# Kernel tuning notes

Hardware: AMD Instinct MI355X
Metric: run time of the kernel (lower is better)

Reference implementation:

```python
import jax, jax.numpy as jnp
import numpy as np

SCALE = 0.08838834764831845  # 1/sqrt(head_dim=128)

T, H, D = 8192, 16, 128
NUM_SLOTS = 16384
SEQ_LEN = 2048


def setup_inputs() -> dict:
    key = jax.random.key(0)
    kq, kk, kv = jax.random.split(key, 3)
    q = jax.random.normal(kq, (T, H, D), dtype=jnp.float32)
    k = jax.random.normal(kk, (T, H, D), dtype=jnp.float32)
    v = jax.random.normal(kv, (T, H, D), dtype=jnp.float32)
    k_cache = jnp.zeros((NUM_SLOTS, H * D), dtype=jnp.float32)
    v_cache = jnp.zeros((NUM_SLOTS, H * D), dtype=jnp.float32)
    slot_mapping = jnp.arange(T, dtype=jnp.int32)  # contiguous slots; -1 would mean skip
    return {"q": q, "k": k, "v": v, "k_cache": k_cache, "v_cache": v_cache,
            "slot_mapping": slot_mapping, "seq_len": SEQ_LEN}


def reference(q, k, v, k_cache, v_cache, slot_mapping, seq_len):
    # --- store_kvcache: scatter per-token K/V rows into paged cache slots ---
    t, h, d = q.shape
    num_slots = k_cache.shape[0]
    # slot == -1 means "do not store"; remap to an out-of-bounds index and drop.
    safe_slots = jnp.where(slot_mapping < 0, num_slots, slot_mapping)
    k_cache = k_cache.at[safe_slots].set(k.reshape(t, h * d), mode="drop")
    v_cache = v_cache.at[safe_slots].set(v.reshape(t, h * d), mode="drop")

    # --- prefill attention reading K/V from the cache (block_tables path) ---
    # cu_seqlens = [0, S, 2S, ...]: equal-length sequences packed contiguously,
    # so the per-sequence cache slices are the first t rows reshaped to [B,S,H,D].
    b = t // seq_len
    qb = q.reshape(b, seq_len, h, d)
    kb = k_cache[:t].reshape(b, seq_len, h, d)
    vb = v_cache[:t].reshape(b, seq_len, h, d)

    scores = jnp.einsum("bqhd,bkhd->bhqk", qb, kb) * SCALE  # [B,H,S,S]
    causal = jnp.tril(jnp.ones((seq_len, seq_len), dtype=bool))
    scores = jnp.where(causal[None, None], scores, -jnp.inf)
    p = jax.nn.softmax(scores, axis=-1)
    o = jnp.einsum("bhqk,bkhd->bqhd", p, vb)
    return o.reshape(t, h, d)
```

## Files before the change

kernel.cpp:

```cpp
#include <hip/hip_runtime.h>

typedef float f32x16 __attribute__((ext_vector_type(16)));
typedef __bf16 bf16x8 __attribute__((ext_vector_type(8)));
typedef unsigned int uint2v __attribute__((ext_vector_type(2)));

#define Hh 16
#define Dd 128
#define SEQ 2048
#define HD 2048
#define ATT_C 0.12751743f
#define NEGINF (-__builtin_inff())

__device__ __forceinline__ ushort f2bf(float f) {
    uint u = __builtin_bit_cast(uint, f);
    return (ushort)((u + 0x7FFFu + ((u >> 16) & 1u)) >> 16);
}

__device__ __forceinline__ uint4 pack8(float4 a, float4 b) {
    uint4 u;
    u.x = (uint)f2bf(a.x) | ((uint)f2bf(a.y) << 16);
    u.y = (uint)f2bf(a.z) | ((uint)f2bf(a.w) << 16);
    u.z = (uint)f2bf(b.x) | ((uint)f2bf(b.y) << 16);
    u.w = (uint)f2bf(b.z) | ((uint)f2bf(b.w) << 16);
    return u;
}

__device__ __forceinline__ uint cvtpk(float a, float b) {
    uint r;
    asm("v_cvt_pk_bf16_f32 %0, %1, %2" : "=v"(r) : "v"(a), "v"(b));
    return r;
}

__device__ __forceinline__ f32x16 zero16() {
    f32x16 v;
#pragma unroll
    for (int i = 0; i < 16; ++i) v[i] = 0.f;
    return v;
}

__device__ __forceinline__ float hsum16(const f32x16 v) {
    float a0 = v[0] + v[1], a1 = v[2] + v[3], a2 = v[4] + v[5], a3 = v[6] + v[7];
    float a4 = v[8] + v[9], a5 = v[10] + v[11], a6 = v[12] + v[13], a7 = v[14] + v[15];
    float b0 = a0 + a1, b1 = a2 + a3, b2 = a4 + a5, b3 = a6 + a7;
    return (b0 + b1) + (b2 + b3);
}

__device__ __forceinline__ void gll16(const void* g, void* l) {
    __builtin_amdgcn_global_load_lds(
        (const __attribute__((address_space(1))) unsigned int*)g,
        (__attribute__((address_space(3))) unsigned int*)l, 16, 0, 0);
}

__device__ __forceinline__ bf16x8 mkfrag(uint a01, uint a23, uint a45, uint a67, int hi) {
    uint4 u;
#if __has_builtin(__builtin_amdgcn_permlane32_swap)
    uint2v xz = __builtin_amdgcn_permlane32_swap(a01, a45, false, false);
    uint2v yw = __builtin_amdgcn_permlane32_swap(a23, a67, false, false);
    u.x = xz[0]; u.y = yw[0]; u.z = xz[1]; u.w = yw[1];
    (void)hi;
#else
    uint s01 = __shfl_xor(a01, 32), s23 = __shfl_xor(a23, 32);
    uint s45 = __shfl_xor(a45, 32), s67 = __shfl_xor(a67, 32);
    u.x = hi ? s45 : a01;
    u.y = hi ? s67 : a23;
    u.z = hi ? a45 : s01;
    u.w = hi ? a67 : s23;
#endif
    return __builtin_bit_cast(bf16x8, u);
}

__global__ void buildinv(const int* __restrict__ slots, int* __restrict__ inv, int T) {
    int t = blockIdx.x * 256 + threadIdx.x;
    if (t < T) { int s = slots[t]; if (s >= 0 && s < T) inv[s] = t; }
}

__global__ void fusekv(const float* __restrict__ k, const float* __restrict__ v,
                       const float* __restrict__ kc, const float* __restrict__ vc,
                       const int* __restrict__ inv, ushort* __restrict__ ek,
                       ushort* __restrict__ evt) {
    __shared__ int sv[64];
    __shared__ ushort Ks[64][136];
    __shared__ ushort Lt[128][72];
    const int tid = threadIdx.x;
    const int r0 = blockIdx.x * 64, h = blockIdx.y;
    const int b = r0 >> 11, tok0 = r0 & (SEQ - 1);
    const long tb = ((long)(b * Hh + h) * 32 + (tok0 >> 6)) * 8192;
    if (tid < 64) sv[tid] = inv[r0 + tid];
    __syncthreads();
#pragma unroll
    for (int i = 0; i < 4; ++i) {
        int idx = i * 256 + tid, r = idx >> 4, sg = idx & 15;
        int s = sv[r];
        const float* src = (s >= 0 ? k + (long)s * HD : kc + (long)(r0 + r) * HD) + h * Dd + sg * 8;
        float4 A = *(const float4*)src;
        float4 Bv = *(const float4*)(src + 4);
        *(uint4*)&Ks[r][sg * 8] = pack8(A, Bv);
    }
    const int d = tid & 127, hf2 = tid >> 7;
#pragma unroll
    for (int i = 0; i < 8; ++i) {
        const int t = i * 8 + hf2 * 4;
        ushort wv[4];
#pragma unroll
        for (int jj = 0; jj < 4; ++jj) {
            int s = sv[t + jj];
            const float* sp = (s >= 0 ? v + (long)s * HD : vc + (long)(r0 + t + jj) * HD) + h * Dd + d;
            wv[jj] = f2bf(*sp);
        }
        uint2 u;
        u.x = (uint)wv[0] | ((uint)wv[1] << 16);
        u.y = (uint)wv[2] | ((uint)wv[3] << 16);
        *(uint2*)&Lt[d][t] = u;
    }
    __syncthreads();
#pragma unroll
    for (int i = 0; i < 4; ++i) {
        int c = i * 256 + tid, l = c & 31, j = (c >> 5) & 15, hf = c >> 9;
        *(uint4*)(ek + tb + (long)c * 8) = *(const uint4*)&Ks[hf * 32 + l][j * 8];
    }
#pragma unroll
    for (int i = 0; i < 4; ++i) {
        int c = i * 256 + tid, l = c & 31, ch = (c >> 5) & 7, nt = c >> 8;
        *(uint4*)(evt + tb + (long)c * 8) = *(const uint4*)&Lt[nt * 32 + l][ch * 8];
    }
}

#define DOHALF(HH)                                                                         \
  {                                                                                        \
    f32x16 za = zero16(), zb = zero16();                                                   \
    __builtin_amdgcn_s_setprio(1);                                                         \
    _Pragma("unroll")                                                                      \
    for (int kk = 0; kk < 4; ++kk) {                                                       \
      za = __builtin_amdgcn_mfma_f32_32x32x16_bf16(                                        \
          *(const bf16x8*)&Kb[(HH) * 4096 + kk * 512 + koff], qf[kk], za, 0, 0, 0);        \
      zb = __builtin_amdgcn_mfma_f32_32x32x16_bf16(                                        \
          *(const bf16x8*)&Kb[(HH) * 4096 + (kk + 4) * 512 + koff], qf[kk + 4], zb, 0, 0, 0); \
    }                                                                                      \
    __builtin_amdgcn_s_setprio(0);                                                         \
    f32x16 z = za + zb;                                                                    \
    const int kb0 = kv0 + (HH) * 32;                                                       \
    if (kb0 + 31 > qtb) {                                                                  \
      _Pragma("unroll")                                                                    \
      for (int r = 0; r < 16; ++r) {                                                       \
        const int kr = kb0 + ((r & 3) + 8 * (r >> 2) + 4 * hi);                            \
        z[r] = (kr <= qpos) ? z[r] : NEGINF;                                               \
      }                                                                                    \
    }                                                                                      \
    _Pragma("unroll")                                                                      \
    for (int r = 0; r < 16; ++r) z[r] = __builtin_amdgcn_exp2f(z[r]);                      \
    lsum += hsum16(z);                                                                     \
    bf16x8 pa0 = mkfrag(cvtpk(z[0], z[1]), cvtpk(z[2], z[3]),                              \
                        cvtpk(z[4], z[5]), cvtpk(z[6], z[7]), hi);                         \
    bf16x8 pa1 = mkfrag(cvtpk(z[8], z[9]), cvtpk(z[10], z[11]),                            \
                        cvtpk(z[12], z[13]), cvtpk(z[14], z[15]), hi);                     \
    __builtin_amdgcn_s_setprio(1);                                                         \
    _Pragma("unroll")                                                                      \
    for (int nt = 0; nt < 4; ++nt) {                                                       \
      const int vb = nt * 2048 + koff + (HH) * 1024;                                       \
      o[nt] = __builtin_amdgcn_mfma_f32_32x32x16_bf16(pa0, *(const bf16x8*)&Vb[vb], o[nt], 0, 0, 0);       \
      o[nt] = __builtin_amdgcn_mfma_f32_32x32x16_bf16(pa1, *(const bf16x8*)&Vb[vb + 512], o[nt], 0, 0, 0); \
    }                                                                                      \
    __builtin_amdgcn_s_setprio(0);                                                         \
  }

__global__ __launch_bounds__(512) void attn32(const float* __restrict__ q,
                                              const ushort* __restrict__ ek,
                                              const ushort* __restrict__ evt,
                                              float* __restrict__ out) {
    __shared__ ushort KV[2][16384];

    const int tid = threadIdx.x;
    const int w = tid >> 6, lane = tid & 63;
    const int l31 = lane & 31, hi = lane >> 5;
    const int g = blockIdx.x;
    const int bh = g & 63;
    const int jj = 7 - (g >> 6);
    const int b = bh >> 4, h = bh & 15;
    const int ns = 4 * (jj + 1);
    const long kvbase = (long)bh * 32 * 8192;
    const int koff = hi * 256 + l31 * 8;
    const int qtb = jj * 256 + w * 32;
    const int qpos = qtb + l31;

    bf16x8 qf[8];
    {
        const float* qp = q + ((long)(b * SEQ + qtb + l31) * Hh + h) * Dd + hi * 8;
#pragma unroll
        for (int kk = 0; kk < 8; ++kk) {
            float4 A = *(const float4*)(qp + kk * 16);
            float4 Bv = *(const float4*)(qp + kk * 16 + 4);
            A.x *= ATT_C; A.y *= ATT_C; A.z *= ATT_C; A.w *= ATT_C;
            Bv.x *= ATT_C; Bv.y *= ATT_C; Bv.z *= ATT_C; Bv.w *= ATT_C;
            union { uint4 u; bf16x8 v; } cv;
            cv.u = pack8(A, Bv);
            qf[kk] = cv.v;
        }
    }
    auto stage = [&](int nb, int t) {
        const ushort* kg = ek + kvbase + (long)t * 8192 + tid * 8;
        const ushort* vg = evt + kvbase + (long)t * 8192 + tid * 8;
        ushort* kl = &KV[nb][tid * 8];
        ushort* vl = &KV[nb][8192 + tid * 8];
#pragma unroll
        for (int i = 0; i < 2; ++i) {
            gll16(kg + i * 4096, kl + i * 4096);
            gll16(vg + i * 4096, vl + i * 4096);
        }
    };

    f32x16 o[4];
#pragma unroll
    for (int nt = 0; nt < 4; ++nt) o[nt] = zero16();
    float lsum = 0.f;

    stage(0, 0);
    __syncthreads();

    int cur = 0;
    for (int s = 0; s < ns; ++s) {
        if (s + 1 < ns) stage(cur ^ 1, s + 1);
        const int kv0 = s * 64;
        const ushort* Kb = &KV[cur][0];
        const ushort* Vb = &KV[cur][8192];

        if (kv0 <= qtb + 31) {
            DOHALF(0);
            if (kv0 + 32 <= qtb + 31) DOHALF(1);
        }

        __syncthreads();
        cur ^= 1;
    }

    const float lt = lsum + __shfl_xor(lsum, 32);
    const float inv_ = 1.f / lt;
#pragma unroll
    for (int r = 0; r < 16; ++r) {
        const int qr = (r & 3) + 8 * (r >> 2) + 4 * hi;
        const float ivr = __shfl(inv_, qr);
        float* op = out + ((long)(b * SEQ + qtb + qr) * Hh + h) * Dd + l31;
        op[0]  = o[0][r] * ivr;
        op[32] = o[1][r] * ivr;
        op[64] = o[2][r] * ivr;
        op[96] = o[3][r] * ivr;
    }
}

extern "C" void kernel_launch(void* const* d_in, const int* in_sizes, int n_in,
                              void* d_out, int out_size, void* d_ws, size_t ws_size,
                              hipStream_t stream) {
    const float* q = (const float*)d_in[0];
    const float* k = (const float*)d_in[1];
    const float* v = (const float*)d_in[2];
    const float* k_cache = (const float*)d_in[3];
    const float* v_cache = (const float*)d_in[4];
    const int* slot_mapping = (const int*)d_in[5];
    float* out = (float*)d_out;

    const int T = in_sizes[0] / HD;
    (void)n_in; (void)out_size; (void)ws_size;

    ushort* ek = (ushort*)d_ws;
    ushort* evt = ek + (size_t)T * HD;
    int* inv = (int*)(evt + (size_t)T * HD);

    hipMemsetAsync(inv, 0xFF, (size_t)T * sizeof(int), stream);
    buildinv<<<T / 256, 256, 0, stream>>>(slot_mapping, inv, T);
    fusekv<<<dim3(T / 64, Hh), 256, 0, stream>>>(k, v, k_cache, v_cache, inv, ek, evt);
    attn32<<<dim3(512), 512, 0, stream>>>(q, ek, evt, out);
}
```

Baseline: 142.7 us.

## Double KV tile per pipeline stage to 128 keys and interleave block scheduling

Each loop iteration now stages and processes 128 keys (two 64-key subtiles) per double-buffered step instead of 64, halving the number of __syncthreads barriers and stage issues. LDS usage doubles to 128 KB per block, which may reduce occupancy. Block-to-query-tile mapping also changes from strictly heaviest-first to a heavy/light interleave across waves of blocks, to balance the causal workload.

```diff
diff --git a/kernel.cpp b/kernel.cpp
--- a/kernel.cpp
+++ b/kernel.cpp
@@ -125,8 +125,10 @@
     }
 }
 
-#define DOHALF(HH)                                                                         \
+#define DOQ(SUB, HH)                                                                       \
   {                                                                                        \
+    const ushort* Kb = &KV[cur][(SUB) * 16384];                                            \
+    const ushort* Vb = &KV[cur][(SUB) * 16384 + 8192];                                     \
     f32x16 za = zero16(), zb = zero16();                                                   \
     __builtin_amdgcn_s_setprio(1);                                                         \
     _Pragma("unroll")                                                                      \
@@ -138,7 +140,7 @@
     }                                                                                      \
     __builtin_amdgcn_s_setprio(0);                                                         \
     f32x16 z = za + zb;                                                                    \
-    const int kb0 = kv0 + (HH) * 32;                                                       \
+    const int kb0 = kv0 + (SUB) * 64 + (HH) * 32;                                          \
     if (kb0 + 31 > qtb) {                                                                  \
       _Pragma("unroll")                                                                    \
       for (int r = 0; r < 16; ++r) {                                                       \
@@ -167,16 +169,17 @@
                                               const ushort* __restrict__ ek,
                                               const ushort* __restrict__ evt,
                                               float* __restrict__ out) {
-    __shared__ ushort KV[2][16384];
+    __shared__ ushort KV[2][32768];
 
     const int tid = threadIdx.x;
     const int w = tid >> 6, lane = tid & 63;
     const int l31 = lane & 31, hi = lane >> 5;
     const int g = blockIdx.x;
     const int bh = g & 63;
-    const int jj = 7 - (g >> 6);
+    const int u_ = g >> 6;
+    const int jj = (u_ < 4) ? 7 - u_ : u_ - 4;
     const int b = bh >> 4, h = bh & 15;
-    const int ns = 4 * (jj + 1);
+    const int ns = 2 * (jj + 1);
     const long kvbase = (long)bh * 32 * 8192;
     const int koff = hi * 256 + l31 * 8;
     const int qtb = jj * 256 + w * 32;
@@ -191,20 +194,24 @@
             float4 Bv = *(const float4*)(qp + kk * 16 + 4);
             A.x *= ATT_C; A.y *= ATT_C; A.z *= ATT_C; A.w *= ATT_C;
             Bv.x *= ATT_C; Bv.y *= ATT_C; Bv.z *= ATT_C; Bv.w *= ATT_C;
-            union { uint4 u; bf16x8 v; } cv;
-            cv.u = pack8(A, Bv);
+            union { uint4 uu; bf16x8 v; } cv;
+            cv.uu = pack8(A, Bv);
             qf[kk] = cv.v;
         }
     }
-    auto stage = [&](int nb, int t) {
-        const ushort* kg = ek + kvbase + (long)t * 8192 + tid * 8;
-        const ushort* vg = evt + kvbase + (long)t * 8192 + tid * 8;
-        ushort* kl = &KV[nb][tid * 8];
-        ushort* vl = &KV[nb][8192 + tid * 8];
-#pragma unroll
-        for (int i = 0; i < 2; ++i) {
-            gll16(kg + i * 4096, kl + i * 4096);
-            gll16(vg + i * 4096, vl + i * 4096);
+    auto stage = [&](int nb, int sp) {
+        const long tbase = kvbase + (long)sp * 16384;
+#pragma unroll
+        for (int sub = 0; sub < 2; ++sub) {
+            const ushort* kg = ek + tbase + sub * 8192 + tid * 8;
+            const ushort* vg = evt + tbase + sub * 8192 + tid * 8;
+            ushort* kl = &KV[nb][sub * 16384 + tid * 8];
+            ushort* vl = &KV[nb][sub * 16384 + 8192 + tid * 8];
+#pragma unroll
+            for (int i = 0; i < 2; ++i) {
+                gll16(kg + i * 4096, kl + i * 4096);
+                gll16(vg + i * 4096, vl + i * 4096);
+            }
         }
     };
 
@@ -219,13 +226,15 @@
     int cur = 0;
     for (int s = 0; s < ns; ++s) {
         if (s + 1 < ns) stage(cur ^ 1, s + 1);
-        const int kv0 = s * 64;
-        const ushort* Kb = &KV[cur][0];
-        const ushort* Vb = &KV[cur][8192];
+        const int kv0 = s * 128;
 
         if (kv0 <= qtb + 31) {
-            DOHALF(0);
-            if (kv0 + 32 <= qtb + 31) DOHALF(1);
+            DOQ(0, 0);
+            if (kv0 + 32 <= qtb + 31) DOQ(0, 1);
+            if (kv0 + 64 <= qtb + 31) {
+                DOQ(1, 0);
+                if (kv0 + 96 <= qtb + 31) DOQ(1, 1);
+            }
         }
 
         __syncthreads();
```

After: 157.3 us. +10.2%, slower.

## Split KV tile across warp pairs and halve query tile per block

Applied to the files above, without the earlier changes.

Each block now handles 128 query rows instead of 256, with the 8 warps split into 4 query sub-tiles times 2 KV halves of each 64-key stage. The two partial outputs and row sums are combined through shared memory at the end. This doubles the grid to 1024 blocks to improve load balance and occupancy across CUs for the causal triangle, at the cost of an extra shared-memory reduction and reloading K/V tiles in more blocks.

```diff
diff --git a/kernel.cpp b/kernel.cpp
--- a/kernel.cpp
+++ b/kernel.cpp
@@ -125,62 +125,28 @@
     }
 }
 
-#define DOHALF(HH)                                                                         \
-  {                                                                                        \
-    f32x16 za = zero16(), zb = zero16();                                                   \
-    __builtin_amdgcn_s_setprio(1);                                                         \
-    _Pragma("unroll")                                                                      \
-    for (int kk = 0; kk < 4; ++kk) {                                                       \
-      za = __builtin_amdgcn_mfma_f32_32x32x16_bf16(                                        \
-          *(const bf16x8*)&Kb[(HH) * 4096 + kk * 512 + koff], qf[kk], za, 0, 0, 0);        \
-      zb = __builtin_amdgcn_mfma_f32_32x32x16_bf16(                                        \
-          *(const bf16x8*)&Kb[(HH) * 4096 + (kk + 4) * 512 + koff], qf[kk + 4], zb, 0, 0, 0); \
-    }                                                                                      \
-    __builtin_amdgcn_s_setprio(0);                                                         \
-    f32x16 z = za + zb;                                                                    \
-    const int kb0 = kv0 + (HH) * 32;                                                       \
-    if (kb0 + 31 > qtb) {                                                                  \
-      _Pragma("unroll")                                                                    \
-      for (int r = 0; r < 16; ++r) {                                                       \
-        const int kr = kb0 + ((r & 3) + 8 * (r >> 2) + 4 * hi);                            \
-        z[r] = (kr <= qpos) ? z[r] : NEGINF;                                               \
-      }                                                                                    \
-    }                                                                                      \
-    _Pragma("unroll")                                                                      \
-    for (int r = 0; r < 16; ++r) z[r] = __builtin_amdgcn_exp2f(z[r]);                      \
-    lsum += hsum16(z);                                                                     \
-    bf16x8 pa0 = mkfrag(cvtpk(z[0], z[1]), cvtpk(z[2], z[3]),                              \
-                        cvtpk(z[4], z[5]), cvtpk(z[6], z[7]), hi);                         \
-    bf16x8 pa1 = mkfrag(cvtpk(z[8], z[9]), cvtpk(z[10], z[11]),                            \
-                        cvtpk(z[12], z[13]), cvtpk(z[14], z[15]), hi);                     \
-    __builtin_amdgcn_s_setprio(1);                                                         \
-    _Pragma("unroll")                                                                      \
-    for (int nt = 0; nt < 4; ++nt) {                                                       \
-      const int vb = nt * 2048 + koff + (HH) * 1024;                                       \
-      o[nt] = __builtin_amdgcn_mfma_f32_32x32x16_bf16(pa0, *(const bf16x8*)&Vb[vb], o[nt], 0, 0, 0);       \
-      o[nt] = __builtin_amdgcn_mfma_f32_32x32x16_bf16(pa1, *(const bf16x8*)&Vb[vb + 512], o[nt], 0, 0, 0); \
-    }                                                                                      \
-    __builtin_amdgcn_s_setprio(0);                                                         \
-  }
-
 __global__ __launch_bounds__(512) void attn32(const float* __restrict__ q,
                                               const ushort* __restrict__ ek,
                                               const ushort* __restrict__ evt,
                                               float* __restrict__ out) {
     __shared__ ushort KV[2][16384];
+    __shared__ float Lsum[64];
 
     const int tid = threadIdx.x;
     const int w = tid >> 6, lane = tid & 63;
     const int l31 = lane & 31, hi = lane >> 5;
+    const int qsub = w & 3, kh = w >> 2;
     const int g = blockIdx.x;
     const int bh = g & 63;
-    const int jj = 7 - (g >> 6);
+    const int t = 15 - (g >> 6);
     const int b = bh >> 4, h = bh & 15;
-    const int ns = 4 * (jj + 1);
+    const int ns = 2 * (t + 1);
     const long kvbase = (long)bh * 32 * 8192;
     const int koff = hi * 256 + l31 * 8;
-    const int qtb = jj * 256 + w * 32;
+    const int qtb = t * 128 + qsub * 32;
     const int qpos = qtb + l31;
+    const int kof2 = kh * 4096;
+    const int vof2 = kh * 1024;
 
     bf16x8 qf[8];
     {
@@ -196,9 +162,9 @@
             qf[kk] = cv.v;
         }
     }
-    auto stage = [&](int nb, int t) {
-        const ushort* kg = ek + kvbase + (long)t * 8192 + tid * 8;
-        const ushort* vg = evt + kvbase + (long)t * 8192 + tid * 8;
+    auto stage = [&](int nb, int ti) {
+        const ushort* kg = ek + kvbase + (long)ti * 8192 + tid * 8;
+        const ushort* vg = evt + kvbase + (long)ti * 8192 + tid * 8;
         ushort* kl = &KV[nb][tid * 8];
         ushort* vl = &KV[nb][8192 + tid * 8];
 #pragma unroll
@@ -220,12 +186,46 @@
     for (int s = 0; s < ns; ++s) {
         if (s + 1 < ns) stage(cur ^ 1, s + 1);
         const int kv0 = s * 64;
-        const ushort* Kb = &KV[cur][0];
+        const ushort* Kb = &KV[cur][kof2];
         const ushort* Vb = &KV[cur][8192];
 
-        if (kv0 <= qtb + 31) {
-            DOHALF(0);
-            if (kv0 + 32 <= qtb + 31) DOHALF(1);
+        if (kv0 + kh * 32 <= qtb + 31) {
+            f32x16 za = zero16(), zb = zero16();
+            __builtin_amdgcn_s_setprio(1);
+#pragma unroll
+            for (int kk = 0; kk < 4; ++kk) {
+                za = __builtin_amdgcn_mfma_f32_32x32x16_bf16(
+                    *(const bf16x8*)&Kb[kk * 512 + koff], qf[kk], za, 0, 0, 0);
+                zb = __builtin_amdgcn_mfma_f32_32x32x16_bf16(
+                    *(const bf16x8*)&Kb[(kk + 4) * 512 + koff], qf[kk + 4], zb, 0, 0, 0);
+            }
+            __builtin_amdgcn_s_setprio(0);
+            f32x16 z = za + zb;
+            const int kb0 = kv0 + kh * 32;
+            if (kb0 + 31 > qtb) {
+#pragma unroll
+                for (int r = 0; r < 16; ++r) {
+                    const int kr = kb0 + ((r & 3) + 8 * (r >> 2) + 4 * hi);
+                    z[r] = (kr <= qpos) ? z[r] : NEGINF;
+                }
+            }
+#pragma unroll
+            for (int r = 0; r < 16; ++r) z[r] = __builtin_amdgcn_exp2f(z[r]);
+            lsum += hsum16(z);
+            bf16x8 pa0 = mkfrag(cvtpk(z[0], z[1]), cvtpk(z[2], z[3]),
+                                cvtpk(z[4], z[5]), cvtpk(z[6], z[7]), hi);
+            bf16x8 pa1 = mkfrag(cvtpk(z[8], z[9]), cvtpk(z[10], z[11]),
+                                cvtpk(z[12], z[13]), cvtpk(z[14], z[15]), hi);
+            __builtin_amdgcn_s_setprio(1);
+#pragma unroll
+            for (int nt = 0; nt < 4; ++nt) {
+                const int vb = nt * 2048 + koff + vof2;
+                o[nt] = __builtin_amdgcn_mfma_f32_32x32x16_bf16(
+                    pa0, *(const bf16x8*)&Vb[vb], o[nt], 0, 0, 0);
+                o[nt] = __builtin_amdgcn_mfma_f32_32x32x16_bf16(
+                    pa1, *(const bf16x8*)&Vb[vb + 512], o[nt], 0, 0, 0);
+            }
+            __builtin_amdgcn_s_setprio(0);
         }
 
         __syncthreads();
@@ -233,16 +233,34 @@
     }
 
     const float lt = lsum + __shfl_xor(lsum, 32);
-    const float inv_ = 1.f / lt;
-#pragma unroll
-    for (int r = 0; r < 16; ++r) {
-        const int qr = (r & 3) + 8 * (r >> 2) + 4 * hi;
-        const float ivr = __shfl(inv_, qr);
-        float* op = out + ((long)(b * SEQ + qtb + qr) * Hh + h) * Dd + l31;
-        op[0]  = o[0][r] * ivr;
-        op[32] = o[1][r] * ivr;
-        op[64] = o[2][r] * ivr;
-        op[96] = o[3][r] * ivr;
+    float* Ox = (float*)&KV[0][0];
+#pragma unroll
+    for (int ph = 0; ph < 2; ++ph) {
+        __syncthreads();
+        if (kh == 1 && (qsub >> 1) == ph) {
+            float* dst = Ox + (qsub & 1) * 4096 + lane;
+#pragma unroll
+            for (int nt = 0; nt < 4; ++nt)
+#pragma unroll
+                for (int r = 0; r < 16; ++r) dst[(nt * 16 + r) * 64] = o[nt][r];
+            if (lane < 32) Lsum[(qsub & 1) * 32 + lane] = lt;
+        }
+        __syncthreads();
+        if (kh == 0 && (qsub >> 1) == ph) {
+            const float* src = Ox + (qsub & 1) * 4096 + lane;
+            const float lt1 = Lsum[(qsub & 1) * 32 + l31];
+            const float inv_ = 1.f / (lt + lt1);
+#pragma unroll
+            for (int r = 0; r < 16; ++r) {
+                const int qr = (r & 3) + 8 * (r >> 2) + 4 * hi;
+                const float ivr = __shfl(inv_, qr);
+                float* op = out + ((long)(b * SEQ + qtb + qr) * Hh + h) * Dd + l31;
+                op[0]  = (o[0][r] + src[(0 * 16 + r) * 64]) * ivr;
+                op[32] = (o[1][r] + src[(1 * 16 + r) * 64]) * ivr;
+                op[64] = (o[2][r] + src[(2 * 16 + r) * 64]) * ivr;
+                op[96] = (o[3][r] + src[(3 * 16 + r) * 64]) * ivr;
+            }
+        }
     }
 }
 
@@ -267,5 +285,5 @@
     hipMemsetAsync(inv, 0xFF, (size_t)T * sizeof(int), stream);
     buildinv<<<T / 256, 256, 0, stream>>>(slot_mapping, inv, T);
     fusekv<<<dim3(T / 64, Hh), 256, 0, stream>>>(k, v, k_cache, v_cache, inv, ek, evt);
-    attn32<<<dim3(512), 512, 0, stream>>>(q, ek, evt, out);
-}
+    attn32<<<dim3(1024), 512, 0, stream>>>(q, ek, evt, out);
+}
```

Result: slower. 181.6 us (+27.3%).

## Give each wave two 32-row query tiles to reuse K/V fragments

Applied to the files above, without the earlier changes.

Each wave now handles 64 query rows as two 32-row tiles instead of one, so every K and V fragment read from LDS feeds two MFMAs. Blocks shrink from 512 to 256 threads with launch bounds (256,2), and staging is adjusted so 256 threads still load the same 64-key tile. The aim is to halve LDS reads per MFMA and cut the number of waves sharing each staged tile. In exchange, registers roughly double for Q fragments and accumulators, which can lower occupancy, and causal masking gets coarser per wave, so some work in diagonal blocks is wasted.

```diff
diff --git a/kernel.cpp b/kernel.cpp
--- a/kernel.cpp
+++ b/kernel.cpp
@@ -127,46 +127,57 @@
 
 #define DOHALF(HH)                                                                         \
   {                                                                                        \
-    f32x16 za = zero16(), zb = zero16();                                                   \
+    f32x16 z0 = zero16(), z1 = zero16();                                                   \
     __builtin_amdgcn_s_setprio(1);                                                         \
     _Pragma("unroll")                                                                      \
-    for (int kk = 0; kk < 4; ++kk) {                                                       \
-      za = __builtin_amdgcn_mfma_f32_32x32x16_bf16(                                        \
-          *(const bf16x8*)&Kb[(HH) * 4096 + kk * 512 + koff], qf[kk], za, 0, 0, 0);        \
-      zb = __builtin_amdgcn_mfma_f32_32x32x16_bf16(                                        \
-          *(const bf16x8*)&Kb[(HH) * 4096 + (kk + 4) * 512 + koff], qf[kk + 4], zb, 0, 0, 0); \
+    for (int kk = 0; kk < 8; ++kk) {                                                       \
+      bf16x8 kf = *(const bf16x8*)&Kb[(HH) * 4096 + kk * 512 + koff];                      \
+      z0 = __builtin_amdgcn_mfma_f32_32x32x16_bf16(kf, qf0[kk], z0, 0, 0, 0);              \
+      z1 = __builtin_amdgcn_mfma_f32_32x32x16_bf16(kf, qf1[kk], z1, 0, 0, 0);              \
     }                                                                                      \
     __builtin_amdgcn_s_setprio(0);                                                         \
-    f32x16 z = za + zb;                                                                    \
     const int kb0 = kv0 + (HH) * 32;                                                       \
     if (kb0 + 31 > qtb) {                                                                  \
       _Pragma("unroll")                                                                    \
       for (int r = 0; r < 16; ++r) {                                                       \
         const int kr = kb0 + ((r & 3) + 8 * (r >> 2) + 4 * hi);                            \
-        z[r] = (kr <= qpos) ? z[r] : NEGINF;                                               \
+        z0[r] = (kr <= qp0) ? z0[r] : NEGINF;                                              \
+        z1[r] = (kr <= qp1) ? z1[r] : NEGINF;                                              \
       }                                                                                    \
     }                                                                                      \
     _Pragma("unroll")                                                                      \
-    for (int r = 0; r < 16; ++r) z[r] = __builtin_amdgcn_exp2f(z[r]);                      \
-    lsum += hsum16(z);                                                                     \
-    bf16x8 pa0 = mkfrag(cvtpk(z[0], z[1]), cvtpk(z[2], z[3]),                              \
-                        cvtpk(z[4], z[5]), cvtpk(z[6], z[7]), hi);                         \
-    bf16x8 pa1 = mkfrag(cvtpk(z[8], z[9]), cvtpk(z[10], z[11]),                            \
-                        cvtpk(z[12], z[13]), cvtpk(z[14], z[15]), hi);                     \
+    for (int r = 0; r < 16; ++r) {                                                         \
+      z0[r] = __builtin_amdgcn_exp2f(z0[r]);                                               \
+      z1[r] = __builtin_amdgcn_exp2f(z1[r]);                                               \
+    }                                                                                      \
+    ls0 += hsum16(z0);                                                                     \
+    ls1 += hsum16(z1);                                                                     \
+    bf16x8 pa00 = mkfrag(cvtpk(z0[0], z0[1]), cvtpk(z0[2], z0[3]),                         \
+                         cvtpk(z0[4], z0[5]), cvtpk(z0[6], z0[7]), hi);                    \
+    bf16x8 pa01 = mkfrag(cvtpk(z0[8], z0[9]), cvtpk(z0[10], z0[11]),                       \
+                         cvtpk(z0[12], z0[13]), cvtpk(z0[14], z0[15]), hi);                \
+    bf16x8 pa10 = mkfrag(cvtpk(z1[0], z1[1]), cvtpk(z1[2], z1[3]),                         \
+                         cvtpk(z1[4], z1[5]), cvtpk(z1[6], z1[7]), hi);                    \
+    bf16x8 pa11 = mkfrag(cvtpk(z1[8], z1[9]), cvtpk(z1[10], z1[11]),                       \
+                         cvtpk(z1[12], z1[13]), cvtpk(z1[14], z1[15]), hi);                \
     __builtin_amdgcn_s_setprio(1);                                                         \
     _Pragma("unroll")                                                                      \
     for (int nt = 0; nt < 4; ++nt) {                                                       \
       const int vb = nt * 2048 + koff + (HH) * 1024;                                       \
-      o[nt] = __builtin_amdgcn_mfma_f32_32x32x16_bf16(pa0, *(const bf16x8*)&Vb[vb], o[nt], 0, 0, 0);       \
-      o[nt] = __builtin_amdgcn_mfma_f32_32x32x16_bf16(pa1, *(const bf16x8*)&Vb[vb + 512], o[nt], 0, 0, 0); \
+      bf16x8 vf0 = *(const bf16x8*)&Vb[vb];                                                \
+      bf16x8 vf1 = *(const bf16x8*)&Vb[vb + 512];                                          \
+      o[nt]     = __builtin_amdgcn_mfma_f32_32x32x16_bf16(pa00, vf0, o[nt], 0, 0, 0);      \
+      o[nt]     = __builtin_amdgcn_mfma_f32_32x32x16_bf16(pa01, vf1, o[nt], 0, 0, 0);      \
+      o[4 + nt] = __builtin_amdgcn_mfma_f32_32x32x16_bf16(pa10, vf0, o[4 + nt], 0, 0, 0);  \
+      o[4 + nt] = __builtin_amdgcn_mfma_f32_32x32x16_bf16(pa11, vf1, o[4 + nt], 0, 0, 0);  \
     }                                                                                      \
     __builtin_amdgcn_s_setprio(0);                                                         \
   }
 
-__global__ __launch_bounds__(512) void attn32(const float* __restrict__ q,
-                                              const ushort* __restrict__ ek,
-                                              const ushort* __restrict__ evt,
-                                              float* __restrict__ out) {
+__global__ __launch_bounds__(256, 2) void attn32(const float* __restrict__ q,
+                                                 const ushort* __restrict__ ek,
+                                                 const ushort* __restrict__ evt,
+                                                 float* __restrict__ out) {
     __shared__ ushort KV[2][16384];
 
     const int tid = threadIdx.x;
@@ -179,12 +190,12 @@
     const int ns = 4 * (jj + 1);
     const long kvbase = (long)bh * 32 * 8192;
     const int koff = hi * 256 + l31 * 8;
-    const int qtb = jj * 256 + w * 32;
-    const int qpos = qtb + l31;
-
-    bf16x8 qf[8];
-    {
-        const float* qp = q + ((long)(b * SEQ + qtb + l31) * Hh + h) * Dd + hi * 8;
+    const int qtb = jj * 256 + w * 64;
+    const int qp0 = qtb + l31, qp1 = qtb + 32 + l31;
+
+    bf16x8 qf0[8], qf1[8];
+    auto loadq = [&](int qrow, bf16x8* qf) {
+        const float* qp = q + ((long)(b * SEQ + qrow) * Hh + h) * Dd + hi * 8;
 #pragma unroll
         for (int kk = 0; kk < 8; ++kk) {
             float4 A = *(const float4*)(qp + kk * 16);
@@ -195,23 +206,26 @@
             cv.u = pack8(A, Bv);
             qf[kk] = cv.v;
         }
-    }
+    };
+    loadq(qtb + l31, qf0);
+    loadq(qtb + 32 + l31, qf1);
+
     auto stage = [&](int nb, int t) {
         const ushort* kg = ek + kvbase + (long)t * 8192 + tid * 8;
         const ushort* vg = evt + kvbase + (long)t * 8192 + tid * 8;
         ushort* kl = &KV[nb][tid * 8];
         ushort* vl = &KV[nb][8192 + tid * 8];
 #pragma unroll
-        for (int i = 0; i < 2; ++i) {
-            gll16(kg + i * 4096, kl + i * 4096);
-            gll16(vg + i * 4096, vl + i * 4096);
+        for (int i = 0; i < 4; ++i) {
+            gll16(kg + i * 2048, kl + i * 2048);
+            gll16(vg + i * 2048, vl + i * 2048);
         }
     };
 
-    f32x16 o[4];
-#pragma unroll
-    for (int nt = 0; nt < 4; ++nt) o[nt] = zero16();
-    float lsum = 0.f;
+    f32x16 o[8];
+#pragma unroll
+    for (int nt = 0; nt < 8; ++nt) o[nt] = zero16();
+    float ls0 = 0.f, ls1 = 0.f;
 
     stage(0, 0);
     __syncthreads();
@@ -223,26 +237,32 @@
         const ushort* Kb = &KV[cur][0];
         const ushort* Vb = &KV[cur][8192];
 
-        if (kv0 <= qtb + 31) {
+        if (kv0 <= qtb + 63) {
             DOHALF(0);
-            if (kv0 + 32 <= qtb + 31) DOHALF(1);
+            if (kv0 + 32 <= qtb + 63) DOHALF(1);
         }
 
         __syncthreads();
         cur ^= 1;
     }
 
-    const float lt = lsum + __shfl_xor(lsum, 32);
-    const float inv_ = 1.f / lt;
+    const float lt0 = ls0 + __shfl_xor(ls0, 32);
+    const float lt1 = ls1 + __shfl_xor(ls1, 32);
+    const float iv0 = 1.f / lt0, iv1 = 1.f / lt1;
 #pragma unroll
     for (int r = 0; r < 16; ++r) {
         const int qr = (r & 3) + 8 * (r >> 2) + 4 * hi;
-        const float ivr = __shfl(inv_, qr);
-        float* op = out + ((long)(b * SEQ + qtb + qr) * Hh + h) * Dd + l31;
-        op[0]  = o[0][r] * ivr;
-        op[32] = o[1][r] * ivr;
-        op[64] = o[2][r] * ivr;
-        op[96] = o[3][r] * ivr;
+        const float a0 = __shfl(iv0, qr), a1 = __shfl(iv1, qr);
+        float* op0 = out + ((long)(b * SEQ + qtb + qr) * Hh + h) * Dd + l31;
+        float* op1 = out + ((long)(b * SEQ + qtb + 32 + qr) * Hh + h) * Dd + l31;
+        op0[0]  = o[0][r] * a0;
+        op0[32] = o[1][r] * a0;
+        op0[64] = o[2][r] * a0;
+        op0[96] = o[3][r] * a0;
+        op1[0]  = o[4][r] * a1;
+        op1[32] = o[5][r] * a1;
+        op1[64] = o[6][r] * a1;
+        op1[96] = o[7][r] * a1;
     }
 }
 
@@ -264,8 +284,8 @@
     ushort* evt = ek + (size_t)T * HD;
     int* inv = (int*)(evt + (size_t)T * HD);
 
-    hipMemsetAsync(inv, 0xFF, (size_t)T * sizeof(int), stream);
+    (void)hipMemsetAsync(inv, 0xFF, (size_t)T * sizeof(int), stream);
     buildinv<<<T / 256, 256, 0, stream>>>(slot_mapping, inv, T);
     fusekv<<<dim3(T / 64, Hh), 256, 0, stream>>>(k, v, k_cache, v_cache, inv, ek, evt);
-    attn32<<<dim3(512), 512, 0, stream>>>(q, ek, evt, out);
-}
+    attn32<<<dim3(512), 256, 0, stream>>>(q, ek, evt, out);
+}
```

Measured after the change: 151.4 us. 6.1% more time.
